# Optimization experiments

Hardware: AMD Instinct MI355X
Metric: run time of the kernel (lower is better)

## Reference

```python
import jax, jax.numpy as jnp
import numpy as np

B = 4096
STATE_DIM = 64
OBS_DIM = 32
BASE_DEGREE = 8
TIME_STEPS = 96
EPS = 1e-7


def _degree(t):
    # get_degree: degree_params initialized to linspace(0,1,time_steps); used via .item() (static)
    p = float(t) / (TIME_STEPS - 1)
    scaled = 0.5 * (1.0 + np.sin(2.0 * np.pi * p))
    return BASE_DEGREE + int(2.0 * scaled)


def _cheby_fwd_and_jac(x, coeffs, degree):
    """ChebyKAN forward y[b,o] = sum_{i,d} coeffs[i,o,d] * cos(d*acos(clip(tanh(x[b,i]))))
    plus its analytic per-sample Jacobian J[b,o,i] (replaces the torch autograd loop)."""
    t_raw = jnp.tanh(x)                                   # [B, D]
    t_val = jnp.clip(t_raw, -1.0 + EPS, 1.0 - EPS)
    theta = jnp.arccos(t_val)                             # [B, D]
    dvals = jnp.arange(degree + 1, dtype=x.dtype)         # [deg+1]
    ang = theta[..., None] * dvals                        # [B, D, deg+1]
    cheb = jnp.cos(ang)
    ac = coeffs[..., : degree + 1]                        # [D, D, deg+1]
    y = jnp.einsum('bid,iod->bo', cheb, ac)               # [B, D]
    # d cheb / d x = d*sin(d*theta) * (1 - tanh(x)^2) * mask / sqrt(1 - t_val^2)
    mask = ((t_raw > -1.0 + EPS) & (t_raw < 1.0 - EPS)).astype(x.dtype)
    dtheta_dx = -(1.0 - t_raw * t_raw) * mask / jnp.sqrt(1.0 - t_val * t_val)  # [B, D]
    dcheb_dx = -dvals * jnp.sin(ang) * dtheta_dx[..., None]                    # [B, D, deg+1]
    jac = jnp.einsum('bid,iod->boi', dcheb_dx, ac)        # [B, D, D] = dY_o/dx_i
    return y, jac


def setup_inputs() -> dict:
    key = jax.random.key(0)
    ks = jax.random.split(key, 5)
    obs = jax.random.normal(ks[0], (B, OBS_DIM), jnp.float32)
    prev_state = jax.random.normal(ks[1], (B, STATE_DIM), jnp.float32)
    A = jax.random.normal(ks[2], (B, STATE_DIM, STATE_DIM), jnp.float32)
    prev_cov = A @ A.transpose(0, 2, 1) / STATE_DIM + jnp.eye(STATE_DIM, dtype=jnp.float32)  # SPD
    bound = 1.0 / np.sqrt(STATE_DIM * (BASE_DEGREE + 3))  # kaiming-uniform style
    coeffs = jax.random.uniform(ks[3], (STATE_DIM, STATE_DIM, BASE_DEGREE + 3), jnp.float32, -bound, bound)
    M = jax.random.normal(ks[4], (STATE_DIM, OBS_DIM), jnp.float32)
    q, _ = jnp.linalg.qr(M)                               # orthonormal columns
    obs_matrix = q.T.astype(jnp.float32)                  # [OBS_DIM, STATE_DIM], orthogonal rows
    log_Q_diag = jnp.zeros((STATE_DIM,), jnp.float32)
    log_R_diag = jnp.zeros((OBS_DIM,), jnp.float32)
    return dict(obs=obs, prev_state=prev_state, prev_cov=prev_cov, coeffs=coeffs,
                obs_matrix=obs_matrix, log_Q_diag=log_Q_diag, log_R_diag=log_R_diag, t=10)


def reference(obs, prev_state, prev_cov, coeffs, obs_matrix, log_Q_diag, log_R_diag, t):
    degree = _degree(t)
    state_pred, Fj = _cheby_fwd_and_jac(prev_state, coeffs, degree)   # [B,D], [B,D,D]
    q = jnp.exp(log_Q_diag)                                           # [D]
    r = jnp.exp(log_R_diag)                                           # [O]
    H = obs_matrix                                                    # [O, D]
    # cov_pred = F P F^T + Q
    cov_pred = jnp.einsum('bij,bjk,blk->bil', Fj, prev_cov, Fj) + jnp.diag(q)[None]
    obs_pred = state_pred @ H.T                                       # [B, O]
    residual = obs - obs_pred                                         # [B, O]
    # S = H Pp H^T + R
    S = jnp.einsum('ij,bjk,lk->bil', H, cov_pred, H) + jnp.diag(r)[None]
    S_inv = jnp.linalg.pinv(S)                                        # [B, O, O]
    PHt = jnp.einsum('bij,oj->bio', cov_pred, H)                      # [B, D, O]
    K = jnp.einsum('bio,bop->bip', PHt, S_inv)                        # [B, D, O]
    state_update = state_pred + jnp.einsum('bio,bo->bi', K, residual)
    I_KH = jnp.eye(STATE_DIM, dtype=cov_pred.dtype)[None] - jnp.einsum('bio,oj->bij', K, H)
    # Joseph form: (I-KH) Pp (I-KH)^T + K R K^T
    cov_update = (jnp.einsum('bij,bjk,blk->bil', I_KH, cov_pred, I_KH)
                  + jnp.einsum('bio,o,bjo->bij', K, r, K))
    cov_diag = jnp.diagonal(cov_update, axis1=1, axis2=2)
    return state_update, cov_update, cov_diag
```

## Files before the change

kernel.cpp:

```cpp
#include <hip/hip_runtime.h>
#include <math.h>


typedef float f4 __attribute__((ext_vector_type(4)));
typedef float f32x4 __attribute__((ext_vector_type(4)));
typedef short b16x8 __attribute__((ext_vector_type(8)));
typedef short b16x4 __attribute__((ext_vector_type(4)));
typedef unsigned int u32;
typedef unsigned int u32x4 __attribute__((ext_vector_type(4)));
typedef unsigned short u16;

#define EPSC 1e-7f
#define MFMA(a, b, c) __builtin_amdgcn_mfma_f32_16x16x32_bf16(a, b, c, 0, 0, 0)
static constexpr size_t CU_OFF = 4096 * 64;
static constexpr size_t CD_OFF = CU_OFF + 4096ull * 4096;

__device__ __forceinline__ void split2(float x, short &h, short &l) {
  u32 u = __float_as_uint(x);
  h = (short)(u >> 16);
  float rem = x - __uint_as_float(u & 0xffff0000u);
  l = (short)(__float_as_uint(rem) >> 16);
}
__device__ __forceinline__ u32 packsplit(float x) {
  u32 u = __float_as_uint(x) & 0xffff0000u;
  float rem = x - __uint_as_float(u);
  return u | (__float_as_uint(rem) >> 16);
}
__device__ __forceinline__ float unpackf(u32 v) {
  return __uint_as_float(v & 0xffff0000u) + __uint_as_float(v << 16);
}
union U8 { u32x4 u; b16x8 s; };
__device__ __forceinline__ void unpack8(u32x4 q0, u32x4 q1, b16x8 &hi,
                                        b16x8 &lo) {
  U8 H, L;
  H.u[0] = __builtin_amdgcn_perm(q0[1], q0[0], 0x07060302u);
  H.u[1] = __builtin_amdgcn_perm(q0[3], q0[2], 0x07060302u);
  H.u[2] = __builtin_amdgcn_perm(q1[1], q1[0], 0x07060302u);
  H.u[3] = __builtin_amdgcn_perm(q1[3], q1[2], 0x07060302u);
  L.u[0] = __builtin_amdgcn_perm(q0[1], q0[0], 0x05040100u);
  L.u[1] = __builtin_amdgcn_perm(q0[3], q0[2], 0x05040100u);
  L.u[2] = __builtin_amdgcn_perm(q1[1], q1[0], 0x05040100u);
  L.u[3] = __builtin_amdgcn_perm(q1[3], q1[2], 0x05040100u);
  hi = H.s;
  lo = L.s;
}
__device__ __forceinline__ void split8v(f4 a, f4 b, b16x8 &hi, b16x8 &lo) {
#pragma unroll
  for (int j = 0; j < 4; ++j) {
    short hh, ll;
    split2(a[j], hh, ll); hi[j] = hh; lo[j] = ll;
    split2(b[j], hh, ll); hi[4 + j] = hh; lo[4 + j] = ll;
  }
}

__global__ __launch_bounds__(256, 4) void kalman_fused(
    const float *__restrict__ obs, const float *__restrict__ prev_state,
    const float *__restrict__ prev_cov, const float *__restrict__ coeffs,
    const float *__restrict__ Hm, const float *__restrict__ logQ,
    const float *__restrict__ logR, const int *__restrict__ tptr,
    float *__restrict__ out) {
  __shared__ __align__(16) unsigned char pool[38144];
  u16 *sPh = (u16 *)(pool);
  u16 *sPl = (u16 *)(pool + 8192);
  u32 *sT = (u32 *)(pool);
  u32 *sPHt = (u32 *)(pool);
  u32 *sK = (u32 *)(pool + 8192);
  u16 *sFh = (u16 *)(pool + 16384);
  u16 *sFl = (u16 *)(pool + 24576);
  u32 *sCov = (u32 *)(pool + 16384);
  float *sS = (float *)(pool + 32768);
  float *ypart = (float *)(pool + 32768);
  float *sTv = (float *)(pool + 33792);
  float *sSn = (float *)(pool + 34048);
  float *sDth = (float *)(pool + 34304);
  float *sy = (float *)(pool + 37376);
  float *sresid = (float *)(pool + 37632);
  float *sq = (float *)(pool + 37760);
  float *sr = (float *)(pool + 38016);

  const int tid = (int)threadIdx.x;
  const int b = (int)blockIdx.x;
  const int w = tid >> 6;
  const int l = tid & 63;
  const int lr = l & 15;
  const int h = l >> 4;

  const int tval = tptr[0];
  const float ang = 6.28318530717958647f * ((float)tval / 95.0f);
  const int D = 9 + (int)(1.0f + sinf(ang));

  {
    const float *Pg = prev_cov + (size_t)b * 4096;
#pragma unroll
    for (int e = 0; e < 4; ++e) {
      const int idx = tid + 256 * e;
      f4 v = *(const f4 *)(Pg + 4 * idx);
      const int r = idx >> 4, c = (idx & 15) * 4;
      const int x = (r & 7) << 3;
      b16x4 h4, l4;
#pragma unroll
      for (int j = 0; j < 4; ++j) {
        short hh, ll;
        split2(v[j], hh, ll);
        h4[j] = hh; l4[j] = ll;
      }
      *(b16x4 *)(sPh + r * 64 + (c ^ x)) = h4;
      *(b16x4 *)(sPl + r * 64 + (c ^ x)) = l4;
    }
    if (tid < 64) {
      sq[tid] = expf(logQ[tid]);
      const float xx = prev_state[b * 64 + tid];
      const float tr_ = tanhf(xx);
      const float tv = fminf(fmaxf(tr_, -1.0f + EPSC), 1.0f - EPSC);
      const float sn = sqrtf(fmaxf(1.0f - tv * tv, 0.0f));
      const float mask = (tr_ > -1.0f + EPSC && tr_ < 1.0f - EPSC) ? 1.0f : 0.0f;
      sTv[tid] = tv;
      sSn[tid] = sn;
      sDth[tid] = -(1.0f - tr_ * tr_) * mask / sn;
    } else if (tid < 96) {
      sr[tid - 64] = expf(logR[tid - 64]);
    }
  }
  __syncthreads();

  {
    const int o = tid & 63, g = tid >> 6;
    float yacc = 0.f;
    float fr[16];
#pragma unroll
    for (int ii = 0; ii < 16; ++ii) {
      const int i = g * 16 + ii;
      const float tv = sTv[i], sn = sSn[i], dth = sDth[i];
      const float *cp = coeffs + (size_t)(i * 64 + o) * 11;
      f4 q0 = *(const f4 *)(cp);
      f4 q1 = *(const f4 *)(cp + 4);
      f4 q2 = *(const f4 *)(cp + 7);
      float cy[11];
#pragma unroll
      for (int j = 0; j < 4; ++j) { cy[j] = q0[j]; cy[4 + j] = q1[j]; }
      cy[8] = q2[1]; cy[9] = q2[2]; cy[10] = q2[3];
      if (D < 10) cy[9] = 0.f;
      if (D < 11) cy[10] = 0.f;
      float yac = fmaf(cy[1], tv, cy[0]);
      float wac = cy[1] * sn;
      float cm2 = 1.f, cm1 = tv, sm2 = 0.f, sm1 = sn;
      const float tv2 = 2.f * tv;
#pragma unroll
      for (int d = 2; d <= 10; ++d) {
        const float cc = fmaf(tv2, cm1, -cm2);
        const float ss = fmaf(tv2, sm1, -sm2);
        yac = fmaf(cy[d], cc, yac);
        wac = fmaf(cy[d] * (float)d, ss, wac);
        cm2 = cm1; cm1 = cc; sm2 = sm1; sm1 = ss;
      }
      yacc += yac;
      fr[ii] = -dth * wac;
    }
    b16x8 fh0, fh1, fl0, fl1;
#pragma unroll
    for (int j = 0; j < 8; ++j) {
      short hh, ll;
      split2(fr[j], hh, ll); fh0[j] = hh; fl0[j] = ll;
      split2(fr[8 + j], hh, ll); fh1[j] = hh; fl1[j] = ll;
    }
    const int x = (o & 7) << 3;
    *(b16x8 *)(sFh + o * 64 + ((g * 16) ^ x)) = fh0;
    *(b16x8 *)(sFh + o * 64 + ((g * 16 + 8) ^ x)) = fh1;
    *(b16x8 *)(sFl + o * 64 + ((g * 16) ^ x)) = fl0;
    *(b16x8 *)(sFl + o * 64 + ((g * 16 + 8) ^ x)) = fl1;
    ypart[g * 64 + o] = yacc;
  }
  __syncthreads();
  if (tid < 64)
    sy[tid] = ypart[tid] + ypart[64 + tid] + ypart[128 + tid] + ypart[192 + tid];
  __syncthreads();

  if (tid < 32) {
    float racc = obs[b * 32 + tid];
    const float *Hr = Hm + tid * 64;
#pragma unroll
    for (int s = 0; s < 64; s += 4) {
      f4 hv = *(const f4 *)(Hr + s);
      racc -= hv[0] * sy[s] + hv[1] * sy[s + 1] + hv[2] * sy[s + 2] +
              hv[3] * sy[s + 3];
    }
    sresid[tid] = racc;
  }

  f32x4 accT[4] = {{0.f, 0.f, 0.f, 0.f}, {0.f, 0.f, 0.f, 0.f},
                   {0.f, 0.f, 0.f, 0.f}, {0.f, 0.f, 0.f, 0.f}};
  {
    const int m = 16 * w + lr;
    const int xA = (m & 7) << 3;
#pragma unroll
    for (int kc = 0; kc < 2; ++kc) {
      const int k = kc * 32 + h * 8;
      b16x8 Ah = *(const b16x8 *)(sFh + m * 64 + (k ^ xA));
      b16x8 Al = *(const b16x8 *)(sFl + m * 64 + (k ^ xA));
#pragma unroll
      for (int t = 0; t < 4; ++t) {
        const int n = t * 16 + lr;
        const int xB = (n & 7) << 3;
        b16x8 Bh = *(const b16x8 *)(sPh + n * 64 + (k ^ xB));
        b16x8 Bl = *(const b16x8 *)(sPl + n * 64 + (k ^ xB));
        accT[t] = MFMA(Ah, Bh, accT[t]);
        accT[t] = MFMA(Al, Bh, accT[t]);
        accT[t] = MFMA(Ah, Bl, accT[t]);
      }
    }
  }
  __syncthreads();
  {
    const int r0 = 16 * w + h * 4;
#pragma unroll
    for (int t = 0; t < 4; ++t)
#pragma unroll
      for (int j = 0; j < 4; ++j) {
        const int rr = r0 + j, cc = t * 16 + lr;
        sT[rr * 64 + (cc ^ ((rr & 7) << 2))] = packsplit(accT[t][j]);
      }
  }

  f32x4 accC[4] = {{0.f, 0.f, 0.f, 0.f}, {0.f, 0.f, 0.f, 0.f},
                   {0.f, 0.f, 0.f, 0.f}, {0.f, 0.f, 0.f, 0.f}};
  {
    const int m = 16 * w + lr;
    const int xA = (m & 7) << 2;
    const u32 *Tb = sT + m * 64;
#pragma unroll
    for (int kc = 0; kc < 2; ++kc) {
      const int k = kc * 32 + h * 8;
      u32x4 q0 = *(const u32x4 *)(Tb + (k ^ xA));
      u32x4 q1 = *(const u32x4 *)(Tb + ((k + 4) ^ xA));
      b16x8 Ah, Al;
      unpack8(q0, q1, Ah, Al);
#pragma unroll
      for (int t = 0; t < 4; ++t) {
        const int n = t * 16 + lr;
        const int xB = (n & 7) << 3;
        b16x8 Bh = *(const b16x8 *)(sFh + n * 64 + (k ^ xB));
        b16x8 Bl = *(const b16x8 *)(sFl + n * 64 + (k ^ xB));
        accC[t] = MFMA(Ah, Bh, accC[t]);
        accC[t] = MFMA(Al, Bh, accC[t]);
        accC[t] = MFMA(Ah, Bl, accC[t]);
      }
    }
  }
  __syncthreads();
  {
    const int r0 = 16 * w + h * 4;
#pragma unroll
    for (int t = 0; t < 4; ++t)
#pragma unroll
      for (int j = 0; j < 4; ++j) {
        const int rr = r0 + j, cc = t * 16 + lr;
        float v = accC[t][j];
        if (rr == cc) v += sq[rr];
        sCov[rr * 64 + (cc ^ ((rr & 7) << 2))] = packsplit(v);
      }
  }

  {
    f32x4 acc[2] = {{0.f, 0.f, 0.f, 0.f}, {0.f, 0.f, 0.f, 0.f}};
    const int m = 16 * w + lr;
    const int xA = (m & 7) << 2;
    const u32 *Cb = sCov + m * 64;
#pragma unroll
    for (int kc = 0; kc < 2; ++kc) {
      const int k = kc * 32 + h * 8;
      u32x4 q0 = *(const u32x4 *)(Cb + (k ^ xA));
      u32x4 q1 = *(const u32x4 *)(Cb + ((k + 4) ^ xA));
      b16x8 Ah, Al;
      unpack8(q0, q1, Ah, Al);
#pragma unroll
      for (int t = 0; t < 2; ++t) {
        const int n = t * 16 + lr;
        const float *Hr = Hm + n * 64 + k;
        f4 b0 = *(const f4 *)(Hr);
        f4 b1 = *(const f4 *)(Hr + 4);
        b16x8 Bh, Bl;
        split8v(b0, b1, Bh, Bl);
        acc[t] = MFMA(Ah, Bh, acc[t]);
        acc[t] = MFMA(Al, Bh, acc[t]);
        acc[t] = MFMA(Ah, Bl, acc[t]);
      }
    }
    const int r0 = 16 * w + h * 4;
#pragma unroll
    for (int t = 0; t < 2; ++t)
#pragma unroll
      for (int j = 0; j < 4; ++j) {
        const int rr = r0 + j, cc = t * 16 + lr;
        sPHt[rr * 32 + (cc ^ ((rr & 7) << 2))] = packsplit(acc[t][j]);
      }
  }
  __syncthreads();

  {
    const int tr = w >> 1, tc = w & 1;
    f32x4 acc = {0.f, 0.f, 0.f, 0.f};
    const int m = tr * 16 + lr;
    const int n = tc * 16 + lr;
#pragma unroll
    for (int kc = 0; kc < 2; ++kc) {
      const int k = kc * 32 + h * 8;
      const float *Hr = Hm + m * 64 + k;
      f4 a0 = *(const f4 *)(Hr);
      f4 a1 = *(const f4 *)(Hr + 4);
      b16x8 Ah, Al;
      split8v(a0, a1, Ah, Al);
      u32x4 q0, q1;
#pragma unroll
      for (int j = 0; j < 4; ++j)
        q0[j] = sPHt[(k + j) * 32 + (n ^ (j << 2))];
#pragma unroll
      for (int j = 0; j < 4; ++j)
        q1[j] = sPHt[(k + 4 + j) * 32 + (n ^ ((4 + j) << 2))];
      b16x8 Bh, Bl;
      unpack8(q0, q1, Bh, Bl);
      acc = MFMA(Ah, Bh, acc);
      acc = MFMA(Al, Bh, acc);
      acc = MFMA(Ah, Bl, acc);
    }
    const int r0 = tr * 16 + h * 4;
#pragma unroll
    for (int j = 0; j < 4; ++j) {
      const int rr = r0 + j, cc = tc * 16 + lr;
      float v = acc[j];
      if (rr == cc) v += sr[rr];
      sS[rr * 36 + cc] = v;
    }
  }
  __syncthreads();

  if (w == 0) {
    const int mr = l >> 1, half = l & 1;
    float s0[16];
    const float *gbase = sS + mr * 36 + half * 16;
    {
      f4 v0 = *(const f4 *)(gbase + 0), v1 = *(const f4 *)(gbase + 4);
      f4 v2 = *(const f4 *)(gbase + 8), v3 = *(const f4 *)(gbase + 12);
#pragma unroll
      for (int j = 0; j < 4; ++j) {
        s0[j] = v0[j]; s0[4 + j] = v1[j]; s0[8 + j] = v2[j]; s0[12 + j] = v3[j];
      }
    }
#pragma unroll
    for (int p = 0; p < 32; ++p) {
      const int ph = p >> 4, pi = p & 15;
      float prow[16];
#pragma unroll
      for (int j = 0; j < 16; ++j) prow[j] = __shfl(s0[j], 2 * p + half, 64);
      const float dpp = __shfl(s0[pi], 2 * p + ph, 64);
      const float d = 1.0f / dpp;
      const float fv = __shfl(s0[pi], (l & 62) + ph, 64);
      if (mr == p) {
#pragma unroll
        for (int j = 0; j < 16; ++j) s0[j] = prow[j] * d;
        if (half == ph) s0[pi] = d;
      } else {
        const float fd = fv * d;
#pragma unroll
        for (int j = 0; j < 16; ++j) s0[j] = fmaf(-fd, prow[j], s0[j]);
        if (half == ph) s0[pi] = -fd;
      }
    }
    float *wbase = sS + mr * 36 + half * 16;
    f4 w0 = {s0[0], s0[1], s0[2], s0[3]};
    f4 w1 = {s0[4], s0[5], s0[6], s0[7]};
    f4 w2 = {s0[8], s0[9], s0[10], s0[11]};
    f4 w3 = {s0[12], s0[13], s0[14], s0[15]};
    *(f4 *)(wbase + 0) = w0;
    *(f4 *)(wbase + 4) = w1;
    *(f4 *)(wbase + 8) = w2;
    *(f4 *)(wbase + 12) = w3;
  }
  __syncthreads();

  {
    f32x4 acc[2] = {{0.f, 0.f, 0.f, 0.f}, {0.f, 0.f, 0.f, 0.f}};
    const int m = 16 * w + lr;
    const int xA = (m & 7) << 2;
    const int k = h * 8;
    u32x4 q0 = *(const u32x4 *)(sPHt + m * 32 + (k ^ xA));
    u32x4 q1 = *(const u32x4 *)(sPHt + m * 32 + ((k + 4) ^ xA));
    b16x8 Ah, Al;
    unpack8(q0, q1, Ah, Al);
#pragma unroll
    for (int t = 0; t < 2; ++t) {
      const int n = t * 16 + lr;
      f4 b0 = *(const f4 *)(sS + n * 36 + k);
      f4 b1 = *(const f4 *)(sS + n * 36 + k + 4);
      b16x8 Bh, Bl;
      split8v(b0, b1, Bh, Bl);
      acc[t] = MFMA(Ah, Bh, acc[t]);
      acc[t] = MFMA(Al, Bh, acc[t]);
      acc[t] = MFMA(Ah, Bl, acc[t]);
    }
    const int r0 = 16 * w + h * 4;
#pragma unroll
    for (int t = 0; t < 2; ++t)
#pragma unroll
      for (int j = 0; j < 4; ++j) {
        const int rr = r0 + j, cc = t * 16 + lr;
        sK[rr * 32 + (cc ^ ((rr & 7) << 2))] = packsplit(acc[t][j]);
      }
  }
  __syncthreads();

  if (tid < 64) {
    float su = sy[tid];
    const int x = (tid & 7) << 2;
    const u32 *Kb = sK + tid * 32;
#pragma unroll
    for (int c0 = 0; c0 < 32; c0 += 4) {
      u32x4 q = *(const u32x4 *)(Kb + (c0 ^ x));
#pragma unroll
      for (int j = 0; j < 4; ++j)
        su = fmaf(unpackf(q[j]), sresid[c0 + j], su);
    }
    out[b * 64 + tid] = su;
  }
  {
    const int m = 16 * w + lr;
    const int xA = (m & 7) << 2;
    const int k = h * 8;
    u32x4 q0 = *(const u32x4 *)(sK + m * 32 + (k ^ xA));
    u32x4 q1 = *(const u32x4 *)(sK + m * 32 + ((k + 4) ^ xA));
#pragma unroll
    for (int j = 0; j < 4; ++j) {
      q0[j] ^= 0x80008000u;
      q1[j] ^= 0x80008000u;
    }
    b16x8 Ah, Al;
    unpack8(q0, q1, Ah, Al);
    const int r0 = 16 * w + h * 4;
    float *outc = out + CU_OFF + (size_t)b * 4096;
#pragma unroll
    for (int t = 0; t < 4; ++t) {
      const int n = t * 16 + lr;
      const int xB = (n & 7) << 2;
      u32x4 p0 = *(const u32x4 *)(sPHt + n * 32 + (k ^ xB));
      u32x4 p1 = *(const u32x4 *)(sPHt + n * 32 + ((k + 4) ^ xB));
      b16x8 Bh, Bl;
      unpack8(p0, p1, Bh, Bl);
      f32x4 acc;
#pragma unroll
      for (int j = 0; j < 4; ++j) {
        const int rr = r0 + j;
        acc[j] = unpackf(sCov[rr * 64 + (n ^ ((rr & 7) << 2))]);
      }
      acc = MFMA(Ah, Bh, acc);
      acc = MFMA(Al, Bh, acc);
      acc = MFMA(Ah, Bl, acc);
#pragma unroll
      for (int j = 0; j < 4; ++j) {
        const int rr = r0 + j;
        outc[rr * 64 + n] = acc[j];
        if (rr == n) out[CD_OFF + b * 64 + rr] = acc[j];
      }
    }
  }
}

extern "C" void kernel_launch(void *const *d_in, const int *in_sizes, int n_in,
                              void *d_out, int out_size, void *d_ws,
                              size_t ws_size, hipStream_t stream) {
  const float *obs = (const float *)d_in[0];
  const float *prev_state = (const float *)d_in[1];
  const float *prev_cov = (const float *)d_in[2];
  const float *coeffs = (const float *)d_in[3];
  const float *Hm = (const float *)d_in[4];
  const float *logQ = (const float *)d_in[5];
  const float *logR = (const float *)d_in[6];
  const int *tptr = (const int *)d_in[7];
  (void)in_sizes; (void)n_in; (void)out_size; (void)d_ws; (void)ws_size;
  kalman_fused<<<dim3(4096), dim3(256), 0, stream>>>(
      obs, prev_state, prev_cov, coeffs, Hm, logQ, logR, tptr, (float *)d_out);
}
```

Measured before the change: 115.8 us.

## Precompute Chebyshev basis per input and pre-split H in a prep kernel

The Chebyshev value and derivative recurrences were recomputed for every (input, output) pair. They are now computed once per input dimension into shared-memory tables, with the degree mask folded in, so the coefficient stage becomes plain FMA dot products. A small prep kernel splits H into bf16 hi/lo halves and exponentiates logQ/logR once into the workspace, which removes per-block split and exp work. One block barrier is replaced by a wave barrier because the producer and consumer threads sit in the same wave. The costs are an extra kernel launch, a dependency on the workspace buffer, and more shared memory, which could affect occupancy.

```diff
diff --git a/kernel.cpp b/kernel.cpp
--- a/kernel.cpp
+++ b/kernel.cpp
@@ -53,13 +53,30 @@
   }
 }
 
+__global__ __launch_bounds__(256) void prep_kernel(
+    const float *__restrict__ Hm, const float *__restrict__ logQ,
+    const float *__restrict__ logR, void *__restrict__ ws) {
+  u16 *Hh = (u16 *)ws;
+  u16 *Hl = (u16 *)ws + 2048;
+  float *wq = (float *)((char *)ws + 8192);
+  float *wr = wq + 64;
+  const int tid = (int)threadIdx.x;
+  f4 a = *(const f4 *)(Hm + tid * 8);
+  f4 b = *(const f4 *)(Hm + tid * 8 + 4);
+  b16x8 hi, lo;
+  split8v(a, b, hi, lo);
+  *(b16x8 *)(Hh + tid * 8) = hi;
+  *(b16x8 *)(Hl + tid * 8) = lo;
+  if (tid < 64) wq[tid] = expf(logQ[tid]);
+  else if (tid < 96) wr[tid - 64] = expf(logR[tid - 64]);
+}
+
 __global__ __launch_bounds__(256, 4) void kalman_fused(
     const float *__restrict__ obs, const float *__restrict__ prev_state,
     const float *__restrict__ prev_cov, const float *__restrict__ coeffs,
-    const float *__restrict__ Hm, const float *__restrict__ logQ,
-    const float *__restrict__ logR, const int *__restrict__ tptr,
-    float *__restrict__ out) {
-  __shared__ __align__(16) unsigned char pool[38144];
+    const float *__restrict__ Hm, const int *__restrict__ tptr,
+    const void *__restrict__ ws, float *__restrict__ out) {
+  __shared__ __align__(16) unsigned char pool[40704];
   u16 *sPh = (u16 *)(pool);
   u16 *sPl = (u16 *)(pool + 8192);
   u32 *sT = (u32 *)(pool);
@@ -68,15 +85,19 @@
   u16 *sFh = (u16 *)(pool + 16384);
   u16 *sFl = (u16 *)(pool + 24576);
   u32 *sCov = (u32 *)(pool + 16384);
+  float *ypart = (float *)(pool + 32768);
   float *sS = (float *)(pool + 32768);
-  float *ypart = (float *)(pool + 32768);
-  float *sTv = (float *)(pool + 33792);
-  float *sSn = (float *)(pool + 34048);
-  float *sDth = (float *)(pool + 34304);
-  float *sy = (float *)(pool + 37376);
-  float *sresid = (float *)(pool + 37632);
-  float *sq = (float *)(pool + 37760);
-  float *sr = (float *)(pool + 38016);
+  float *sChT = (float *)(pool + 33792);
+  float *sDcT = (float *)(pool + 36864);
+  float *sy = (float *)(pool + 39936);
+  float *sresid = (float *)(pool + 40192);
+  float *sq = (float *)(pool + 40320);
+  float *sr = (float *)(pool + 40576);
+
+  const u16 *wHh = (const u16 *)ws;
+  const u16 *wHl = (const u16 *)ws + 2048;
+  const float *wq = (const float *)((const char *)ws + 8192);
+  const float *wr = wq + 64;
 
   const int tid = (int)threadIdx.x;
   const int b = (int)blockIdx.x;
@@ -108,17 +129,29 @@
       *(b16x4 *)(sPl + r * 64 + (c ^ x)) = l4;
     }
     if (tid < 64) {
-      sq[tid] = expf(logQ[tid]);
+      sq[tid] = wq[tid];
       const float xx = prev_state[b * 64 + tid];
       const float tr_ = tanhf(xx);
       const float tv = fminf(fmaxf(tr_, -1.0f + EPSC), 1.0f - EPSC);
       const float sn = sqrtf(fmaxf(1.0f - tv * tv, 0.0f));
       const float mask = (tr_ > -1.0f + EPSC && tr_ < 1.0f - EPSC) ? 1.0f : 0.0f;
-      sTv[tid] = tv;
-      sSn[tid] = sn;
-      sDth[tid] = -(1.0f - tr_ * tr_) * mask / sn;
+      const float dth = -(1.0f - tr_ * tr_) * mask / sn;
+      float *ct = sChT + tid * 12;
+      float *dt = sDcT + tid * 12;
+      ct[0] = 1.f; ct[1] = tv; ct[11] = 0.f;
+      dt[0] = 0.f; dt[1] = -dth * sn; dt[11] = 0.f;
+      float cm2 = 1.f, cm1 = tv, sm2 = 0.f, sm1 = sn;
+      const float tv2 = 2.f * tv;
+#pragma unroll
+      for (int d = 2; d <= 10; ++d) {
+        const float cc = fmaf(tv2, cm1, -cm2);
+        const float ss = fmaf(tv2, sm1, -sm2);
+        ct[d] = (d < D) ? cc : 0.f;
+        dt[d] = (d < D) ? (-dth * (float)d * ss) : 0.f;
+        cm2 = cm1; cm1 = cc; sm2 = sm1; sm1 = ss;
+      }
     } else if (tid < 96) {
-      sr[tid - 64] = expf(logR[tid - 64]);
+      sr[tid - 64] = wr[tid - 64];
     }
   }
   __syncthreads();
@@ -130,31 +163,39 @@
 #pragma unroll
     for (int ii = 0; ii < 16; ++ii) {
       const int i = g * 16 + ii;
-      const float tv = sTv[i], sn = sSn[i], dth = sDth[i];
       const float *cp = coeffs + (size_t)(i * 64 + o) * 11;
       f4 q0 = *(const f4 *)(cp);
       f4 q1 = *(const f4 *)(cp + 4);
       f4 q2 = *(const f4 *)(cp + 7);
-      float cy[11];
-#pragma unroll
-      for (int j = 0; j < 4; ++j) { cy[j] = q0[j]; cy[4 + j] = q1[j]; }
-      cy[8] = q2[1]; cy[9] = q2[2]; cy[10] = q2[3];
-      if (D < 10) cy[9] = 0.f;
-      if (D < 11) cy[10] = 0.f;
-      float yac = fmaf(cy[1], tv, cy[0]);
-      float wac = cy[1] * sn;
-      float cm2 = 1.f, cm1 = tv, sm2 = 0.f, sm1 = sn;
-      const float tv2 = 2.f * tv;
-#pragma unroll
-      for (int d = 2; d <= 10; ++d) {
-        const float cc = fmaf(tv2, cm1, -cm2);
-        const float ss = fmaf(tv2, sm1, -sm2);
-        yac = fmaf(cy[d], cc, yac);
-        wac = fmaf(cy[d] * (float)d, ss, wac);
-        cm2 = cm1; cm1 = cc; sm2 = sm1; sm1 = ss;
-      }
+      const float *ct = sChT + i * 12;
+      const float *dt = sDcT + i * 12;
+      f4 c0 = *(const f4 *)(ct), c1 = *(const f4 *)(ct + 4),
+         c2 = *(const f4 *)(ct + 8);
+      f4 e0 = *(const f4 *)(dt), e1 = *(const f4 *)(dt + 4),
+         e2 = *(const f4 *)(dt + 8);
+      float yac = q0[0];
+      yac = fmaf(q0[1], c0[1], yac);
+      yac = fmaf(q0[2], c0[2], yac);
+      yac = fmaf(q0[3], c0[3], yac);
+      yac = fmaf(q1[0], c1[0], yac);
+      yac = fmaf(q1[1], c1[1], yac);
+      yac = fmaf(q1[2], c1[2], yac);
+      yac = fmaf(q1[3], c1[3], yac);
+      yac = fmaf(q2[1], c2[0], yac);
+      yac = fmaf(q2[2], c2[1], yac);
+      yac = fmaf(q2[3], c2[2], yac);
+      float fra = q0[1] * e0[1];
+      fra = fmaf(q0[2], e0[2], fra);
+      fra = fmaf(q0[3], e0[3], fra);
+      fra = fmaf(q1[0], e1[0], fra);
+      fra = fmaf(q1[1], e1[1], fra);
+      fra = fmaf(q1[2], e1[2], fra);
+      fra = fmaf(q1[3], e1[3], fra);
+      fra = fmaf(q2[1], e2[0], fra);
+      fra = fmaf(q2[2], e2[1], fra);
+      fra = fmaf(q2[3], e2[2], fra);
       yacc += yac;
-      fr[ii] = -dth * wac;
+      fr[ii] = fra;
     }
     b16x8 fh0, fh1, fl0, fl1;
 #pragma unroll
@@ -171,10 +212,12 @@
     ypart[g * 64 + o] = yacc;
   }
   __syncthreads();
-  if (tid < 64)
-    sy[tid] = ypart[tid] + ypart[64 + tid] + ypart[128 + tid] + ypart[192 + tid];
-  __syncthreads();
-
+
+  if (tid < 64) {
+    sy[tid] = ypart[tid] + ypart[64 + tid] + ypart[128 + tid] +
+              ypart[192 + tid];
+  }
+  __builtin_amdgcn_wave_barrier();
   if (tid < 32) {
     float racc = obs[b * 32 + tid];
     const float *Hr = Hm + tid * 64;
@@ -275,11 +318,8 @@
 #pragma unroll
       for (int t = 0; t < 2; ++t) {
         const int n = t * 16 + lr;
-        const float *Hr = Hm + n * 64 + k;
-        f4 b0 = *(const f4 *)(Hr);
-        f4 b1 = *(const f4 *)(Hr + 4);
-        b16x8 Bh, Bl;
-        split8v(b0, b1, Bh, Bl);
+        b16x8 Bh = *(const b16x8 *)(wHh + n * 64 + k);
+        b16x8 Bl = *(const b16x8 *)(wHl + n * 64 + k);
         acc[t] = MFMA(Ah, Bh, acc[t]);
         acc[t] = MFMA(Al, Bh, acc[t]);
         acc[t] = MFMA(Ah, Bl, acc[t]);
@@ -304,11 +344,8 @@
 #pragma unroll
     for (int kc = 0; kc < 2; ++kc) {
       const int k = kc * 32 + h * 8;
-      const float *Hr = Hm + m * 64 + k;
-      f4 a0 = *(const f4 *)(Hr);
-      f4 a1 = *(const f4 *)(Hr + 4);
-      b16x8 Ah, Al;
-      split8v(a0, a1, Ah, Al);
+      b16x8 Ah = *(const b16x8 *)(wHh + m * 64 + k);
+      b16x8 Al = *(const b16x8 *)(wHl + m * 64 + k);
       u32x4 q0, q1;
 #pragma unroll
       for (int j = 0; j < 4; ++j)
@@ -474,7 +511,8 @@
   const float *logQ = (const float *)d_in[5];
   const float *logR = (const float *)d_in[6];
   const int *tptr = (const int *)d_in[7];
-  (void)in_sizes; (void)n_in; (void)out_size; (void)d_ws; (void)ws_size;
+  (void)in_sizes; (void)n_in; (void)out_size; (void)ws_size;
+  prep_kernel<<<dim3(1), dim3(256), 0, stream>>>(Hm, logQ, logR, d_ws);
   kalman_fused<<<dim3(4096), dim3(256), 0, stream>>>(
-      obs, prev_state, prev_cov, coeffs, Hm, logQ, logR, tptr, (float *)d_out);
-}
+      obs, prev_state, prev_cov, coeffs, Hm, tptr, d_ws, (float *)d_out);
+}
```

Measured after the change: 121.1 us. +4.6%, slower.
